# Optimization experiments

Measured on AMD Instinct MI355X. Metric: run time of the kernel, lower is better.

Reference implementation:

```python
import jax, jax.numpy as jnp
import numpy as np

NUM_GROUP, GROUP_SIZE = 128, 32
MASK = (64, 32, 32)
FEAT_DIM, N_POINTS = 1024, 2048
NBR_K = int(1.2 * GROUP_SIZE)  # int(nbr_ratio * group_size) = 38
SUPPORT, NBHD = 8, 32
W_RECON, W_MATCH, W_LATENT, W_MAN = 1.0, 1.0, 1.0, 0.1

gather = jax.vmap(lambda p, i: p[i])  # batched index_points

def sqdist(a, b):  # [B,M,3],[B,N,3] -> [B,M,N]
    return (jnp.sum(a * a, -1)[:, :, None] + jnp.sum(b * b, -1)[:, None, :]
            - 2.0 * jnp.einsum('bmd,bnd->bmn', a, b))

def knn_idx(q, db, k):  # indices into db of k nearest to each query
    return jax.lax.top_k(-sqdist(q, db), k)[1]

def fps(pts, G):  # farthest point sampling, [B,N,3] -> [B,G] indices
    b, n, _ = pts.shape
    def step(carry, _):
        min_d, far = carry
        cur = jnp.take_along_axis(pts, far[:, None, None], axis=1)
        min_d = jnp.minimum(min_d, jnp.sum((pts - cur) ** 2, -1))
        return (min_d, jnp.argmax(min_d, -1).astype(jnp.int32)), far
    init = (jnp.full((b, n), 1e10, dtype=pts.dtype), jnp.zeros((b,), jnp.int32))
    _, idxs = jax.lax.scan(step, init, None, length=G)
    return idxs.T

def bn(h, g, b_, m, v):  # BatchNorm1d, eval-mode running stats
    return (h - m) * jax.lax.rsqrt(v + 1e-5) * g + b_

def chamfer_l1(a, b):
    d = sqdist(a, b)
    d1 = jnp.sqrt(jnp.maximum(jnp.min(d, axis=2), 1e-12))
    d2 = jnp.sqrt(jnp.maximum(jnp.min(d, axis=1), 1e-12))
    return 0.5 * (d1.mean() + d2.mean())

def estimate_normals(xyz, K):  # PCA normal per point + direction disambiguation
    nb = gather(xyz, knn_idx(xyz, xyz, K))          # [B,N,K,3]
    c = nb - nb.mean(axis=2, keepdims=True)
    cov = jnp.einsum('bnki,bnkj->bnij', c, c) / K   # [B,N,3,3]
    _, v = jnp.linalg.eigh(cov)
    n = v[..., 0]                                   # smallest-eigenvalue eigvec
    proj = jnp.einsum('bnkd,bnd->bn', nb - xyz[:, :, None, :], n)
    return n * jnp.where(proj >= 0.0, 1.0, -1.0)[..., None]

def forward_all(pts, W1, b1, g1, be1, m1, v1, W2, b2, W3, b3, g2, be2, m2, v2,
                W4, b4, D1W, D1b, D2W, D2b, D3W, D3b, D4W, D4b):
    bsz = pts.shape[0]
    def encoder(x):  # PCN encoder: pointwise convs + global max pooling
        n = x.shape[1]
        h = jax.nn.relu(bn(x @ W1.T + b1, g1, be1, m1, v1))
        h = h @ W2.T + b2                           # [B,n,256]
        gmax = h.max(axis=1)
        h = jnp.concatenate([jnp.broadcast_to(gmax[:, None, :], (bsz, n, gmax.shape[-1])), h], axis=-1)
        h = jax.nn.relu(bn(h @ W3.T + b3, g2, be2, m2, v2))
        return (h @ W4.T + b4).max(axis=1)          # [B,FEAT_DIM]
    def decoder(z):
        h = jax.nn.relu(z @ D1W.T + D1b)
        h = jax.nn.relu(h @ D2W.T + D2b)
        h = jax.nn.relu(h @ D3W.T + D3b)
        return (h @ D4W.T + D4b).reshape(bsz, -1, 3)
    # --- Group divider: FPS centers + knn neighborhoods (centered) ---
    center = gather(pts, fps(pts, NUM_GROUP))       # [B,G,3]
    nbrs = gather(pts, knn_idx(center, pts, GROUP_SIZE)) - center[:, :, None, :]
    o1, o2 = MASK[0], MASK[0] + MASK[1]             # identity perm partition
    ng = (nbrs[:, :o1], nbrs[:, o1:o2], nbrs[:, o2:])
    cg = (center[:, :o1], center[:, o1:o2], center[:, o2:])
    rebuild0 = (ng[0] + cg[0][:, :, None, :]).reshape(bsz, -1, 3)
    feat = encoder(rebuild0)
    pred = decoder(feat)                            # [B,N_POINTS,3]
    # shape reconstruction loss
    idx = knn_idx(cg[0], pred, NBR_K)
    l_recon = W_RECON * chamfer_l1(rebuild0, gather(pred, idx).reshape(bsz, -1, 3))
    # shape matching loss
    rebuild1 = (ng[1] + cg[1][:, :, None, :]).reshape(bsz, -1, 3)
    idx = knn_idx(cg[1], pred, NBR_K)
    l_match = W_MATCH * chamfer_l1(rebuild1, gather(pred, idx).reshape(bsz, -1, 3))
    # latent reconstruction (detached input) - SmoothL1
    idx = knn_idx(cg[2], pred, GROUP_SIZE)
    feat_recon = encoder(jax.lax.stop_gradient(gather(pred, idx).reshape(bsz, -1, 3)))
    diff = feat - feat_recon
    ad = jnp.abs(diff)
    l_latent = W_LATENT * jnp.where(ad < 1.0, 0.5 * diff * diff, ad - 0.5).mean()
    # manifoldness (normal consistency) constraint
    normals = estimate_normals(pred, NBHD)
    nb = gather(normals, knn_idx(pred, pred, SUPPORT))  # [B,N,8,3]
    a = nb[:, :, :1, :]
    cos = jnp.sum(a * nb, -1) / (jnp.maximum(jnp.linalg.norm(a, axis=-1), 1e-6)
                                 * jnp.maximum(jnp.linalg.norm(nb, axis=-1), 1e-6))
    l_man = W_MAN * jnp.std(1.0 - cos, axis=-1, ddof=1).mean(axis=-1).mean()
    total = l_recon + l_match + l_latent + l_man
    return total, l_recon, l_match, l_latent, l_man


def setup_inputs() -> dict:
    ks = jax.random.split(jax.random.key(0), 10)
    rn = lambda k, sh: jax.random.normal(k, sh, jnp.float32) * 0.02
    z, o = jnp.zeros, jnp.ones
    return dict(
        pts=jax.random.normal(ks[0], (16, 2048, 3), jnp.float32),
        W1=rn(ks[1], (128, 3)), b1=z(128), g1=o(128), be1=z(128), m1=z(128), v1=o(128),
        W2=rn(ks[2], (256, 128)), b2=z(256),
        W3=rn(ks[3], (512, 512)), b3=z(512), g2=o(512), be2=z(512), m2=z(512), v2=o(512),
        W4=rn(ks[4], (FEAT_DIM, 512)), b4=z(FEAT_DIM),
        D1W=rn(ks[5], (2048, FEAT_DIM)), D1b=z(2048),
        D2W=rn(ks[6], (2048, 2048)), D2b=z(2048),
        D3W=rn(ks[7], (2048, 2048)), D3b=z(2048),
        D4W=rn(ks[8], (3 * N_POINTS, 2048)), D4b=z(3 * N_POINTS),
    )


def reference(pts, W1, b1, g1, be1, m1, v1, W2, b2, W3, b3, g2, be2, m2, v2,
              W4, b4, D1W, D1b, D2W, D2b, D3W, D3b, D4W, D4b):
    return forward_all(pts, W1, b1, g1, be1, m1, v1, W2, b2, W3, b3, g2, be2,
                       m2, v2, W4, b4, D1W, D1b, D2W, D2b, D3W, D3b, D4W, D4b)
```

## Files before the change

### kernel.cpp

```cpp
#include <hip/hip_runtime.h>
#include <math.h>

#define BSZ 16
#define NPTS 2048
#define NG 128
#define GS 32
#define NBRK 38

typedef _Float16 f16;
typedef _Float16 f16x8 __attribute__((ext_vector_type(8)));
typedef float f32x4 __attribute__((ext_vector_type(4)));

__device__ __forceinline__ unsigned fkey(float x) {
    unsigned u = __float_as_uint(x);
    return (u >> 31) ? ~u : (u | 0x80000000u);
}
__device__ __forceinline__ float fkey_inv(unsigned k) {
    unsigned u = (k >> 31) ? (k ^ 0x80000000u) : ~k;
    return __uint_as_float(u);
}

__device__ __forceinline__ unsigned wave_min_u32(unsigned v) {
    unsigned t;
    t = (unsigned)__builtin_amdgcn_update_dpp(-1, (int)v, 0x111, 0xF, 0xF, false);
    v = v < t ? v : t;
    t = (unsigned)__builtin_amdgcn_update_dpp(-1, (int)v, 0x112, 0xF, 0xF, false);
    v = v < t ? v : t;
    t = (unsigned)__builtin_amdgcn_update_dpp(-1, (int)v, 0x114, 0xF, 0xF, false);
    v = v < t ? v : t;
    t = (unsigned)__builtin_amdgcn_update_dpp(-1, (int)v, 0x118, 0xF, 0xF, false);
    v = v < t ? v : t;
    t = (unsigned)__builtin_amdgcn_update_dpp(-1, (int)v, 0x142, 0xA, 0xF, false);
    v = v < t ? v : t;
    t = (unsigned)__builtin_amdgcn_update_dpp(-1, (int)v, 0x143, 0xC, 0xF, false);
    v = v < t ? v : t;
    return (unsigned)__builtin_amdgcn_readlane((int)v, 63);
}

__device__ __forceinline__ unsigned long long wave_max_u64(unsigned long long v) {
#define DPPSTEP(ctrl, rmask)                                                                \
    {                                                                                       \
        unsigned tlo = (unsigned)__builtin_amdgcn_update_dpp(0, (int)(unsigned)v, ctrl,     \
                                                             rmask, 0xF, false);            \
        unsigned thi = (unsigned)__builtin_amdgcn_update_dpp(0, (int)(unsigned)(v >> 32),   \
                                                             ctrl, rmask, 0xF, false);      \
        unsigned long long t = ((unsigned long long)thi << 32) | tlo;                       \
        v = t > v ? t : v;                                                                  \
    }
    DPPSTEP(0x111, 0xF)
    DPPSTEP(0x112, 0xF)
    DPPSTEP(0x114, 0xF)
    DPPSTEP(0x118, 0xF)
    DPPSTEP(0x142, 0xA)
    DPPSTEP(0x143, 0xC)
#undef DPPSTEP
    unsigned rlo = (unsigned)__builtin_amdgcn_readlane((int)(unsigned)v, 63);
    unsigned rhi = (unsigned)__builtin_amdgcn_readlane((int)(unsigned)(v >> 32), 63);
    return ((unsigned long long)rhi << 32) | rlo;
}

__global__ __launch_bounds__(256, 1) void fps_kernel_v5(const float* __restrict__ pts,
                                                        float* __restrict__ center) {
    int b = blockIdx.x;
    const float* P = pts + (size_t)b * NPTS * 3;
    int tid = threadIdx.x;
    int lane = tid & 63, wave = tid >> 6;
    __shared__ __align__(16) float Pl[NPTS * 3];
    __shared__ __align__(16) float slot[2][4][8];
#pragma unroll
    for (int i = 0; i < 6; ++i) {
        int v4 = tid + i * 256;
        ((f32x4*)Pl)[v4] = ((const f32x4*)P)[v4];
    }
    __syncthreads();
    float px[8], py[8], pz[8], mind[8];
#pragma unroll
    for (int m = 0; m < 8; ++m) {
        int j = tid + (m << 8);
        px[m] = Pl[j * 3 + 0];
        py[m] = Pl[j * 3 + 1];
        pz[m] = Pl[j * 3 + 2];
        mind[m] = 1e10f;
    }
    float cx = Pl[0], cy = Pl[1], cz = Pl[2];
    float* C = center + (size_t)b * NG * 3;
#pragma unroll 1
    for (int g = 0; g < NG; ++g) {
        if (tid == 0) {
            C[g * 3 + 0] = cx; C[g * 3 + 1] = cy; C[g * 3 + 2] = cz;
        }
        if (g == NG - 1) break;
        float best0 = -1.f, best1 = -1.f;
        int bm0 = 0, bm1 = 1;
#pragma unroll
        for (int m = 0; m < 8; m += 2) {
            float dx0 = px[m] - cx, dy0 = py[m] - cy, dz0 = pz[m] - cz;
            float d0 = dx0 * dx0 + dy0 * dy0 + dz0 * dz0;
            float md0 = fminf(mind[m], d0);
            mind[m] = md0;
            if (md0 > best0) { best0 = md0; bm0 = m; }
            float dx1 = px[m + 1] - cx, dy1 = py[m + 1] - cy, dz1 = pz[m + 1] - cz;
            float d1 = dx1 * dx1 + dy1 * dy1 + dz1 * dz1;
            float md1 = fminf(mind[m + 1], d1);
            mind[m + 1] = md1;
            if (md1 > best1) { best1 = md1; bm1 = m + 1; }
        }
        bool t = (best1 > best0) || (best1 == best0 && bm1 < bm0);
        float bv = t ? best1 : best0;
        int bi = t ? bm1 : bm0;
        unsigned j = (unsigned)(tid + (bi << 8));
        unsigned long long key =
            ((unsigned long long)__float_as_uint(bv) << 32) | (unsigned)(~j);
        key = wave_max_u64(key);
        unsigned bj = ~(unsigned)key;
        int par = g & 1;
        if (lane < 3) slot[par][wave][2 + lane] = Pl[bj * 3 + lane];
        if (lane == 0) {
            slot[par][wave][0] = __uint_as_float((unsigned)key);
            slot[par][wave][1] = __uint_as_float((unsigned)(key >> 32));
        }
        __syncthreads();
        unsigned long long kb = 0ull;
        float nx = 0.f, ny = 0.f, nz = 0.f;
#pragma unroll
        for (int w = 0; w < 4; ++w) {
            f32x4 v = *(const f32x4*)&slot[par][w][0];
            float vz = slot[par][w][4];
            unsigned long long kk =
                ((unsigned long long)__float_as_uint(v[1]) << 32) | __float_as_uint(v[0]);
            bool tw = kk > kb;
            kb = tw ? kk : kb;
            nx = tw ? v[2] : nx;
            ny = tw ? v[3] : ny;
            nz = tw ? vz : nz;
        }
        cx = nx; cy = ny; cz = nz;
    }
}

__device__ __forceinline__ void knn_query(const float* __restrict__ q,
                                          const float* __restrict__ db,
                                          int k, int* __restrict__ o, int lane) {
    const unsigned KINF = 0xFFFFFFFFu;
    float qx = q[0], qy = q[1], qz = q[2];
    float qq = qx * qx + qy * qy + qz * qz;
    unsigned key[32];
    unsigned c0 = KINF, c1 = KINF, c2 = KINF, c3 = KINF;
#pragma unroll
    for (int m = 0; m < 32; ++m) {
        int j = lane + (m << 6);
        float bx = db[j * 3 + 0], by = db[j * 3 + 1], bz = db[j * 3 + 2];
        float dv = qq + bx * bx + by * by + bz * bz - 2.0f * (qx * bx + qy * by + qz * bz);
        unsigned qd = (unsigned)fminf(fmaxf(dv, 0.f) * 8192.0f, 2097151.f);
        unsigned kk = (qd << 11) | (unsigned)j;
        key[m] = kk;
        if (kk < c3) {
            if (kk < c2) {
                c3 = c2;
                if (kk < c1) {
                    c2 = c1;
                    if (kk < c0) { c1 = c0; c0 = kk; } else c1 = kk;
                } else c2 = kk;
            } else c3 = kk;
        }
    }
    unsigned hw = c3;
    int ncached = 4;
    for (int r = 0; r < k; ++r) {
        bool need = (c0 == KINF) && (ncached < 32);
        if (__any(need)) {
            unsigned best = KINF;
#pragma unroll
            for (int m = 0; m < 32; ++m) {
                unsigned v = key[m];
                best = (v > hw && v < best) ? v : best;
            }
            if (need) {
                c0 = best;
                hw = best;
                ncached = (best == KINF) ? 32 : ncached + 1;
            }
        }
        unsigned g = wave_min_u32(c0);
        if (lane == 0) o[r] = (int)(g & 0x7FFu);
        if (((g & 0x7FFu) & 63u) == (unsigned)lane) {
            c0 = c1; c1 = c2; c2 = c3; c3 = KINF;
        }
    }
}

__global__ void knn_kernel_v7(const float* __restrict__ Q, int q_bstride, int q_off, int nq,
                              const float* __restrict__ DB, int k,
                              int* __restrict__ out, int nbatch) {
    int wave = threadIdx.x >> 6, lane = threadIdx.x & 63;
    int qidx = blockIdx.x * 4 + wave;
    if (qidx >= nbatch * nq) return;
    int b = qidx / nq, qi = qidx % nq;
    knn_query(Q + ((size_t)b * q_bstride + q_off + qi) * 3,
              DB + (size_t)b * NPTS * 3, k, out + (size_t)qidx * k, lane);
}

__global__ void knn_post_kernel(const float* __restrict__ center,
                                const float* __restrict__ pred,
                                int* __restrict__ idxa, int* __restrict__ idxb,
                                int* __restrict__ idxc, int* __restrict__ knn32) {
    int wave = threadIdx.x >> 6, lane = threadIdx.x & 63;
    if (blockIdx.x < 512) {
        int qidx = blockIdx.x * 4 + wave;
        int b = qidx >> 7, qi = qidx & 127;
        const float* q = center + ((size_t)b * NG + qi) * 3;
        const float* db = pred + (size_t)b * NPTS * 3;
        int k; int* o;
        if (qi < 64) { k = NBRK; o = idxa + ((size_t)b * 64 + qi) * NBRK; }
        else if (qi < 96) { k = NBRK; o = idxb + ((size_t)b * 32 + qi - 64) * NBRK; }
        else { k = GS; o = idxc + ((size_t)b * 32 + qi - 96) * GS; }
        knn_query(q, db, k, o, lane);
    } else {
        int qidx = (blockIdx.x - 512) * 4 + wave;
        int b = qidx >> 11, qi = qidx & 2047;
        const float* db = pred + (size_t)b * NPTS * 3;
        knn_query(db + (size_t)qi * 3, db, GS, knn32 + (size_t)qidx * GS, lane);
    }
}

__global__ void gather_rebuild_kernel(const float* __restrict__ pts,
                                      const int* __restrict__ knnc,
                                      float* __restrict__ rebuild0,
                                      float* __restrict__ rebuild1) {
    int t = blockIdx.x * 256 + threadIdx.x;
    int s, tt; float* out;
    if (t < BSZ * 2048) {
        tt = t;
        int b = tt >> 11, j = tt & 2047;
        s = knnc[(size_t)b * (NG * GS) + j];
        out = rebuild0;
    } else {
        tt = t - BSZ * 2048;
        int b = tt >> 10, j = tt & 1023;
        s = knnc[(size_t)b * (NG * GS) + 2048 + j];
        out = rebuild1;
    }
    int b2 = (out == rebuild0) ? (tt >> 11) : (tt >> 10);
    const float* p = pts + ((size_t)b2 * NPTS + s) * 3;
    out[(size_t)tt * 3 + 0] = p[0];
    out[(size_t)tt * 3 + 1] = p[1];
    out[(size_t)tt * 3 + 2] = p[2];
}

__global__ void gather_abc_kernel(const float* __restrict__ pred,
                                  const int* __restrict__ idxa,
                                  const int* __restrict__ idxb,
                                  const int* __restrict__ idxc,
                                  float* __restrict__ gatha,
                                  float* __restrict__ gathb,
                                  float* __restrict__ gathc) {
    const int NA = BSZ * 2432, NB_ = BSZ * 1216, NC = BSZ * 1024;
    int t = blockIdx.x * 256 + threadIdx.x;
    const int* idx; int m, tt; float* out;
    if (t < NA) { tt = t; idx = idxa; m = 2432; out = gatha; }
    else if (t < NA + NB_) { tt = t - NA; idx = idxb; m = 1216; out = gathb; }
    else if (t < NA + NB_ + NC) { tt = t - NA - NB_; idx = idxc; m = 1024; out = gathc; }
    else return;
    int b = tt / m, j = tt - b * m;
    int s = idx[(size_t)b * m + j];
    const float* p = pred + ((size_t)b * NPTS + s) * 3;
    out[(size_t)tt * 3 + 0] = p[0];
    out[(size_t)tt * 3 + 1] = p[1];
    out[(size_t)tt * 3 + 2] = p[2];
}

__global__ void cvt_all_kernel(const float* __restrict__ W2, const float* __restrict__ W3,
                               const float* __restrict__ W4, f16* __restrict__ W2h,
                               f16* __restrict__ W3h, f16* __restrict__ W4h) {
    int t = blockIdx.x * 256 + threadIdx.x;
    if (t < 32768) {
        int n = t >> 7, k = t & 127;
        W2h[t] = (f16)W2[(size_t)n * 128 + k];
    } else if (t < 163840) {
        int u = t - 32768;
        int n = u >> 8, k = u & 255;
        W3h[u] = (f16)W3[(size_t)n * 512 + 256 + k];
    } else if (t < 688128) {
        int u = t - 163840;
        int n = u >> 9, k = u & 511;
        W4h[u] = (f16)W4[(size_t)n * 512 + k];
    }
}

__global__ void layer1_kernel(const float* __restrict__ X, const float* __restrict__ W1,
                              const float* __restrict__ b1, const float* __restrict__ g1,
                              const float* __restrict__ be1, const float* __restrict__ m1,
                              const float* __restrict__ v1, f16* __restrict__ H1, int M) {
    __shared__ float w[384], bb[128], sg[128], sb[128], sm[128], sv[128];
    for (int i = threadIdx.x; i < 384; i += 256) w[i] = W1[i];
    if (threadIdx.x < 128) {
        int c = threadIdx.x;
        bb[c] = b1[c]; sg[c] = g1[c]; sb[c] = be1[c]; sm[c] = m1[c]; sv[c] = v1[c];
    }
    __syncthreads();
    int t = blockIdx.x * 256 + threadIdx.x;
    if (t >= M * 16) return;
    int row = t >> 4, cg = (t & 15) * 8;
    float x0 = X[(size_t)row * 3], x1 = X[(size_t)row * 3 + 1], x2 = X[(size_t)row * 3 + 2];
    f16x8 outv;
#pragma unroll
    for (int j = 0; j < 8; ++j) {
        int c = cg + j;
        float tv = x0 * w[c * 3] + x1 * w[c * 3 + 1] + x2 * w[c * 3 + 2] + bb[c];
        float vv = (tv - sm[c]) * rsqrtf(sv[c] + 1e-5f) * sg[c] + sb[c];
        outv[j] = (f16)fmaxf(vv, 0.f);
    }
    *(f16x8*)&H1[(size_t)row * 128 + cg] = outv;
}

__global__ __launch_bounds__(256) void mfma_gemm_kernel(
        const f16* __restrict__ A, const f16* __restrict__ W, int K, int N,
        const float* __restrict__ bias, const float* __restrict__ bias2d,
        const float* __restrict__ bng, const float* __restrict__ bnb,
        const float* __restrict__ bnm, const float* __restrict__ bnv,
        f16* __restrict__ Cout, unsigned* __restrict__ maxkey,
        int rows_per_batch, int relu) {
    __shared__ f16 Als[128 * 40];
    __shared__ f16 Bls[128 * 40];
    int tid = threadIdx.x;
    int lane = tid & 63;
    int wave = tid >> 6;
    int wm = wave & 1, wn = wave >> 1;
    int c16 = lane & 15, quad = lane >> 4;
    int gx = gridDim.x;
    int nwg = gx * gridDim.y;
    int lin = blockIdx.y * gx + blockIdx.x;
    int qc = nwg >> 3, rc = nwg & 7;
    int xcd = lin & 7, pos = lin >> 3;
    int nlin = (xcd < rc ? xcd * (qc + 1) : rc * (qc + 1) + (xcd - rc) * qc) + pos;
    int row0 = (nlin / gx) * 128, col0 = (nlin % gx) * 128;
    int sr = tid >> 2;
    int skc = (tid & 3) * 8;

    f32x4 acc[4][4];
#pragma unroll
    for (int i = 0; i < 4; ++i)
#pragma unroll
        for (int j = 0; j < 4; ++j) acc[i][j] = (f32x4){0.f, 0.f, 0.f, 0.f};

    const f16* Ab = A + (size_t)(row0 + sr) * K + skc;
    const f16* Ab2 = A + (size_t)(row0 + sr + 64) * K + skc;
    const f16* Wb = W + (size_t)(col0 + sr) * K + skc;
    const f16* Wb2 = W + (size_t)(col0 + sr + 64) * K + skc;

    f16x8 pa0 = *(const f16x8*)Ab;
    f16x8 pa1 = *(const f16x8*)Ab2;
    f16x8 pb0 = *(const f16x8*)Wb;
    f16x8 pb1 = *(const f16x8*)Wb2;

    for (int k0 = 0; k0 < K; k0 += 32) {
        *(f16x8*)&Als[sr * 40 + skc] = pa0;
        *(f16x8*)&Als[(sr + 64) * 40 + skc] = pa1;
        *(f16x8*)&Bls[sr * 40 + skc] = pb0;
        *(f16x8*)&Bls[(sr + 64) * 40 + skc] = pb1;
        __syncthreads();
        if (k0 + 32 < K) {
            int kn = k0 + 32;
            pa0 = *(const f16x8*)(Ab + kn);
            pa1 = *(const f16x8*)(Ab2 + kn);
            pb0 = *(const f16x8*)(Wb + kn);
            pb1 = *(const f16x8*)(Wb2 + kn);
        }
        f16x8 af[4], bf[4];
#pragma unroll
        for (int s = 0; s < 4; ++s) {
            af[s] = *(const f16x8*)&Als[(wm * 64 + s * 16 + c16) * 40 + quad * 8];
            bf[s] = *(const f16x8*)&Bls[(wn * 64 + s * 16 + c16) * 40 + quad * 8];
        }
#pragma unroll
        for (int ms = 0; ms < 4; ++ms)
#pragma unroll
            for (int ns = 0; ns < 4; ++ns)
                acc[ms][ns] = __builtin_amdgcn_mfma_f32_16x16x32_f16(af[ms], bf[ns],
                                                                     acc[ms][ns], 0, 0, 0);
        __syncthreads();
    }

    int b = row0 / rows_per_batch;
#pragma unroll
    for (int ns = 0; ns < 4; ++ns) {
        int col = col0 + wn * 64 + ns * 16 + c16;
        float bv = bias ? bias[col] : 0.f;
        float b2v = bias2d ? bias2d[(size_t)b * N + col] : 0.f;
        float mx = -3e38f;
#pragma unroll
        for (int ms = 0; ms < 4; ++ms) {
#pragma unroll
            for (int j = 0; j < 4; ++j) {
                float v = acc[ms][ns][j] + bv + b2v;
                if (bng) v = (v - bnm[col]) * rsqrtf(bnv[col] + 1e-5f) * bng[col] + bnb[col];
                if (relu) v = fmaxf(v, 0.f);
                if (Cout)
                    Cout[(size_t)(row0 + wm * 64 + ms * 16 + quad * 4 + j) * N + col] = (f16)v;
                mx = fmaxf(mx, v);
            }
        }
        if (maxkey) {
            mx = fmaxf(mx, __shfl_xor(mx, 16, 64));
            mx = fmaxf(mx, __shfl_xor(mx, 32, 64));
            if (quad == 0) atomicMax(&maxkey[(size_t)b * N + col], fkey(mx));
        }
    }
}

__global__ void skinny_v2_kernel(const float* __restrict__ A, const float* __restrict__ W,
                                 int ldw, int woff, const float* __restrict__ bias,
                                 float* __restrict__ C, int K, int N, int relu, int akey) {
    int wave = threadIdx.x >> 6, lane = threadIdx.x & 63;
    int col = blockIdx.x * 4 + wave;
    if (col >= N) return;
    const float* w = W + (size_t)col * ldw + woff;
    float acc[16];
#pragma unroll
    for (int m = 0; m < 16; ++m) acc[m] = 0.f;
    for (int k0 = 0; k0 < K; k0 += 256) {
        f32x4 wv = *(const f32x4*)(w + k0 + lane * 4);
#pragma unroll
        for (int m = 0; m < 16; ++m) {
            f32x4 av = *(const f32x4*)(A + (size_t)m * K + k0 + lane * 4);
            if (akey) {
#pragma unroll
                for (int u = 0; u < 4; ++u) av[u] = fkey_inv(__float_as_uint(av[u]));
            }
            acc[m] += av[0] * wv[0] + av[1] * wv[1] + av[2] * wv[2] + av[3] * wv[3];
        }
    }
#pragma unroll
    for (int m = 0; m < 16; ++m)
#pragma unroll
        for (int s = 1; s < 64; s <<= 1) acc[m] += __shfl_xor(acc[m], s, 64);
    if (lane == 0) {
        float bv = bias[col];
#pragma unroll
        for (int m = 0; m < 16; ++m) {
            float v = acc[m] + bv;
            if (relu) v = fmaxf(v, 0.f);
            C[(size_t)m * N + col] = v;
        }
    }
}

__global__ void chamfer4_kernel(const float* __restrict__ rebuild0,
                                const float* __restrict__ gatha,
                                const float* __restrict__ rebuild1,
                                const float* __restrict__ gathb,
                                float* __restrict__ accum) {
    int blk = blockIdx.x;
    const float *A, *Bp; int na, nb, base; float* slot;
    if (blk < 1024)      { A = rebuild0; na = 2048; Bp = gatha;    nb = 2432; slot = accum + 0; base = 0; }
    else if (blk < 2240) { A = gatha;    na = 2432; Bp = rebuild0; nb = 2048; slot = accum + 1; base = 1024; }
    else if (blk < 2752) { A = rebuild1; na = 1024; Bp = gathb;    nb = 1216; slot = accum + 2; base = 2240; }
    else                 { A = gathb;    na = 1216; Bp = rebuild1; nb = 1024; slot = accum + 3; base = 2752; }
    int t = (blk - base) * 256 + threadIdx.x;
    int pt = t >> 3, sl = t & 7;
    float val = 0.f;
    if (pt < BSZ * na) {
        int b = pt / na;
        const float* a = A + (size_t)pt * 3;
        float ax = a[0], ay = a[1], az = a[2];
        float aa = ax * ax + ay * ay + az * az;
        const float* Bb = Bp + (size_t)b * nb * 3;
        float m = 3e38f;
        for (int j = sl; j < nb; j += 8) {
            float bx = Bb[j * 3 + 0], by = Bb[j * 3 + 1], bz = Bb[j * 3 + 2];
            float d = aa + bx * bx + by * by + bz * bz - 2.0f * (ax * bx + ay * by + az * bz);
            m = fminf(m, d);
        }
#pragma unroll
        for (int s = 1; s < 8; s <<= 1) m = fminf(m, __shfl_xor(m, s, 64));
        if (sl == 0) val = sqrtf(fmaxf(m, 1e-12f));
    }
    __shared__ float sdata[256];
    sdata[threadIdx.x] = val;
    __syncthreads();
    for (int s = 128; s > 0; s >>= 1) {
        if (threadIdx.x < s) sdata[threadIdx.x] += sdata[threadIdx.x + s];
        __syncthreads();
    }
    if (threadIdx.x == 0) atomicAdd(slot, sdata[0]);
}

__global__ void latent_kernel(const unsigned* __restrict__ k1,
                              const unsigned* __restrict__ k2,
                              int n, float* __restrict__ slot) {
    int t = blockIdx.x * blockDim.x + threadIdx.x;
    float val = 0.f;
    if (t < n) {
        float d = fkey_inv(k1[t]) - fkey_inv(k2[t]);
        float ad = fabsf(d);
        val = (ad < 1.f) ? (0.5f * d * d) : (ad - 0.5f);
    }
    __shared__ float sdata[256];
    sdata[threadIdx.x] = val;
    __syncthreads();
    for (int s = 128; s > 0; s >>= 1) {
        if (threadIdx.x < s) sdata[threadIdx.x] += sdata[threadIdx.x + s];
        __syncthreads();
    }
    if (threadIdx.x == 0) atomicAdd(slot, sdata[0]);
}

__device__ void smallest_evec(double cxx, double cxy, double cxz,
                              double cyy, double cyz, double czz, double ev[3]) {
    double p1 = cxy * cxy + cxz * cxz + cyz * cyz;
    double q = (cxx + cyy + czz) / 3.0;
    double p2 = (cxx - q) * (cxx - q) + (cyy - q) * (cyy - q) + (czz - q) * (czz - q) + 2.0 * p1;
    double lam = q;
    if (p2 > 0.0) {
        double p = sqrt(p2 / 6.0);
        double b00 = (cxx - q) / p, b11 = (cyy - q) / p, b22 = (czz - q) / p;
        double b01 = cxy / p, b02 = cxz / p, b12 = cyz / p;
        double detB = b00 * (b11 * b22 - b12 * b12) - b01 * (b01 * b22 - b12 * b02)
                    + b02 * (b01 * b12 - b11 * b02);
        double r = detB * 0.5;
        r = r < -1.0 ? -1.0 : (r > 1.0 ? 1.0 : r);
        double phi = acos(r) / 3.0;
        lam = q + 2.0 * p * cos(phi + 2.0943951023931953);
    }
    double r0x = cxx - lam, r0y = cxy, r0z = cxz;
    double r1x = cxy, r1y = cyy - lam, r1z = cyz;
    double r2x = cxz, r2y = cyz, r2z = czz - lam;
    double c0x = r0y * r1z - r0z * r1y, c0y = r0z * r1x - r0x * r1z, c0z = r0x * r1y - r0y * r1x;
    double c1x = r0y * r2z - r0z * r2y, c1y = r0z * r2x - r0x * r2z, c1z = r0x * r2y - r0y * r2x;
    double c2x = r1y * r2z - r1z * r2y, c2y = r1z * r2x - r1x * r2z, c2z = r1x * r2y - r1y * r2x;
    double n0 = c0x * c0x + c0y * c0y + c0z * c0z;
    double n1 = c1x * c1x + c1y * c1y + c1z * c1z;
    double n2 = c2x * c2x + c2y * c2y + c2z * c2z;
    double bx = c0x, by = c0y, bz = c0z, bn = n0;
    if (n1 > bn) { bx = c1x; by = c1y; bz = c1z; bn = n1; }
    if (n2 > bn) { bx = c2x; by = c2y; bz = c2z; bn = n2; }
    if (bn < 1e-280) { ev[0] = 1.0; ev[1] = 0.0; ev[2] = 0.0; return; }
    double inv = 1.0 / sqrt(bn);
    ev[0] = bx * inv; ev[1] = by * inv; ev[2] = bz * inv;
}

__global__ __launch_bounds__(64) void normals_kernel(const float* __restrict__ pred,
                                                     const int* __restrict__ knn,
                                                     float* __restrict__ nrm) {
    int t = blockIdx.x * 64 + threadIdx.x;
    if (t >= BSZ * NPTS) return;
    int b = t / NPTS, i = t % NPTS;
    const float* P = pred + (size_t)b * NPTS * 3;
    const int* id = knn + (size_t)t * 32;
    double sx = 0, sy = 0, sz = 0;
    double sxx = 0, sxy = 0, sxz = 0, syy = 0, syz = 0, szz = 0;
#pragma unroll
    for (int k0 = 0; k0 < 32; k0 += 4) {
        int4 jj = *(const int4*)&id[k0];
#pragma unroll
        for (int u = 0; u < 4; ++u) {
            int j = (u == 0) ? jj.x : (u == 1) ? jj.y : (u == 2) ? jj.z : jj.w;
            double x = (double)P[j * 3 + 0];
            double y = (double)P[j * 3 + 1];
            double z = (double)P[j * 3 + 2];
            sx += x; sy += y; sz += z;
            sxx += x * x; sxy += x * y; sxz += x * z;
            syy += y * y; syz += y * z; szz += z * z;
        }
    }
    double mx = sx * (1.0 / 32.0), my = sy * (1.0 / 32.0), mz = sz * (1.0 / 32.0);
    double cxx = sxx * (1.0 / 32.0) - mx * mx;
    double cxy = sxy * (1.0 / 32.0) - mx * my;
    double cxz = sxz * (1.0 / 32.0) - mx * mz;
    double cyy = syy * (1.0 / 32.0) - my * my;
    double cyz = syz * (1.0 / 32.0) - my * mz;
    double czz = szz * (1.0 / 32.0) - mz * mz;
    double ev[3];
    smallest_evec(cxx, cxy, cxz, cyy, cyz, czz, ev);
    float qx = P[i * 3 + 0], qy = P[i * 3 + 1], qz = P[i * 3 + 2];
    double proj = (sx - 32.0 * (double)qx) * ev[0] + (sy - 32.0 * (double)qy) * ev[1]
                + (sz - 32.0 * (double)qz) * ev[2];
    double s = (proj >= 0.0) ? 1.0 : -1.0;
    nrm[(size_t)t * 3 + 0] = (float)(ev[0] * s);
    nrm[(size_t)t * 3 + 1] = (float)(ev[1] * s);
    nrm[(size_t)t * 3 + 2] = (float)(ev[2] * s);
}

__global__ void manifold_kernel(const float* __restrict__ nrm, const int* __restrict__ knn,
                                int kstride, float* __restrict__ slot) {
    int t = blockIdx.x * blockDim.x + threadIdx.x;
    float val = 0.f;
    if (t < BSZ * NPTS) {
        int b = t / NPTS;
        const float* NB = nrm + (size_t)b * NPTS * 3;
        const int* id = knn + (size_t)t * kstride;
        int j0 = id[0];
        float ax = NB[j0 * 3 + 0], ay = NB[j0 * 3 + 1], az = NB[j0 * 3 + 2];
        float an = fmaxf(sqrtf(ax * ax + ay * ay + az * az), 1e-6f);
        float x[8]; float s = 0.f;
        for (int k = 0; k < 8; ++k) {
            int j = id[k];
            float bx = NB[j * 3 + 0], by = NB[j * 3 + 1], bz = NB[j * 3 + 2];
            float bn_ = fmaxf(sqrtf(bx * bx + by * by + bz * bz), 1e-6f);
            float c = (ax * bx + ay * by + az * bz) / (an * bn_);
            x[k] = 1.f - c; s += x[k];
        }
        float mean = s / 8.f;
        float var = 0.f;
        for (int k = 0; k < 8; ++k) { float d = x[k] - mean; var += d * d; }
        val = sqrtf(var / 7.f);
    }
    __shared__ float sdata[256];
    sdata[threadIdx.x] = val;
    __syncthreads();
    for (int s2 = 128; s2 > 0; s2 >>= 1) {
        if (threadIdx.x < s2) sdata[threadIdx.x] += sdata[threadIdx.x + s2];
        __syncthreads();
    }
    if (threadIdx.x == 0) atomicAdd(slot, sdata[0]);
}

__global__ void finalize_kernel(const float* __restrict__ acc, float* __restrict__ out) {
    float l_recon = 0.5f * (acc[0] / (16.f * 2048.f) + acc[1] / (16.f * 2432.f));
    float l_match = 0.5f * (acc[2] / (16.f * 1024.f) + acc[3] / (16.f * 1216.f));
    float l_latent = acc[4] / (16.f * 1024.f);
    float l_man = 0.1f * (acc[5] / (16.f * 2048.f));
    out[0] = l_recon + l_match + l_latent + l_man;
    out[1] = l_recon;
    out[2] = l_match;
    out[3] = l_latent;
    out[4] = l_man;
}

extern "C" void kernel_launch(void* const* d_in, const int* in_sizes, int n_in,
                              void* d_out, int out_size, void* d_ws, size_t ws_size,
                              hipStream_t stream) {
    (void)in_sizes; (void)n_in; (void)out_size; (void)ws_size;
    const float* pts = (const float*)d_in[0];
    const float* W1 = (const float*)d_in[1];
    const float* b1 = (const float*)d_in[2];
    const float* g1 = (const float*)d_in[3];
    const float* be1 = (const float*)d_in[4];
    const float* m1 = (const float*)d_in[5];
    const float* v1 = (const float*)d_in[6];
    const float* W2 = (const float*)d_in[7];
    const float* b2 = (const float*)d_in[8];
    const float* W3 = (const float*)d_in[9];
    const float* b3 = (const float*)d_in[10];
    const float* g2 = (const float*)d_in[11];
    const float* be2 = (const float*)d_in[12];
    const float* m2 = (const float*)d_in[13];
    const float* v2 = (const float*)d_in[14];
    const float* W4 = (const float*)d_in[15];
    const float* b4 = (const float*)d_in[16];
    const float* D1W = (const float*)d_in[17];
    const float* D1b = (const float*)d_in[18];
    const float* D2W = (const float*)d_in[19];
    const float* D2b = (const float*)d_in[20];
    const float* D3W = (const float*)d_in[21];
    const float* D3b = (const float*)d_in[22];
    const float* D4W = (const float*)d_in[23];
    const float* D4b = (const float*)d_in[24];

    char* ws = (char*)d_ws;
    size_t off = 0;
    auto alloc = [&](size_t bytes) -> void* {
        void* p = ws + off;
        off += (bytes + 255) & ~(size_t)255;
        return p;
    };
    float* center   = (float*)alloc((size_t)BSZ * NG * 3 * 4);
    int*   knnc     = (int*)  alloc((size_t)BSZ * NG * GS * 4);
    float* rebuild0 = (float*)alloc((size_t)BSZ * 2048 * 3 * 4);
    float* rebuild1 = (float*)alloc((size_t)BSZ * 1024 * 3 * 4);
    f16*   W2h      = (f16*)  alloc((size_t)256 * 128 * 2);
    f16*   W3h      = (f16*)  alloc((size_t)512 * 256 * 2);
    f16*   W4h      = (f16*)  alloc((size_t)1024 * 512 * 2);
    f16*   H1h      = (f16*)  alloc((size_t)BSZ * 2048 * 128 * 2);
    f16*   H2h      = (f16*)  alloc((size_t)BSZ * 2048 * 256 * 2);
    f16*   H3h      = (f16*)  alloc((size_t)BSZ * 2048 * 512 * 2);
    unsigned* keybase = (unsigned*)alloc(((size_t)BSZ * 2560 + 64) * 4);
    unsigned* gmaxkey1 = keybase;
    unsigned* gmaxkey2 = keybase + (size_t)BSZ * 256;
    unsigned* featkey1 = keybase + (size_t)BSZ * 512;
    unsigned* featkey2 = keybase + (size_t)BSZ * 512 + (size_t)BSZ * 1024;
    float* accum = (float*)(keybase + (size_t)BSZ * 2560);
    float* gpart    = (float*)alloc((size_t)BSZ * 512 * 4);
    float* dh1      = (float*)alloc((size_t)BSZ * 2048 * 4);
    float* dh2      = (float*)alloc((size_t)BSZ * 2048 * 4);
    float* dh3      = (float*)alloc((size_t)BSZ * 2048 * 4);
    float* pred     = (float*)alloc((size_t)BSZ * 6144 * 4);
    int*   idxa     = (int*)  alloc((size_t)BSZ * 64 * NBRK * 4);
    float* gatha    = (float*)alloc((size_t)BSZ * 64 * NBRK * 3 * 4);
    int*   idxb     = (int*)  alloc((size_t)BSZ * 32 * NBRK * 4);
    float* gathb    = (float*)alloc((size_t)BSZ * 32 * NBRK * 3 * 4);
    int*   idxc     = (int*)  alloc((size_t)BSZ * 32 * 32 * 4);
    float* gathc    = (float*)alloc((size_t)BSZ * 1024 * 3 * 4);
    int*   knn32    = (int*)  alloc((size_t)BSZ * 2048 * 32 * 4);
    float* nrmbuf   = (float*)alloc((size_t)BSZ * 2048 * 3 * 4);

    hipMemsetAsync(keybase, 0, ((size_t)BSZ * 2560 + 8) * 4, stream);

    cvt_all_kernel<<<2688, 256, 0, stream>>>(W2, W3, W4, W2h, W3h, W4h);

    fps_kernel_v5<<<BSZ, 256, 0, stream>>>(pts, center);
    knn_kernel_v7<<<(BSZ * NG + 3) / 4, 256, 0, stream>>>(center, NG, 0, NG, pts, GS,
                                                          knnc, BSZ);
    gather_rebuild_kernel<<<(BSZ * 3072) / 256, 256, 0, stream>>>(pts, knnc,
                                                                  rebuild0, rebuild1);

    auto enc = [&](const float* X, int n, unsigned* gkey, unsigned* fkeyout) {
        int M = BSZ * n;
        layer1_kernel<<<M / 16, 256, 0, stream>>>(X, W1, b1, g1, be1, m1, v1, H1h, M);
        mfma_gemm_kernel<<<dim3(256 / 128, M / 128), 256, 0, stream>>>(
            H1h, W2h, 128, 256, b2, nullptr, nullptr, nullptr, nullptr, nullptr,
            H2h, gkey, n, 0);
        skinny_v2_kernel<<<(512 + 3) / 4, 256, 0, stream>>>(
            (const float*)gkey, W3, 512, 0, b3, gpart, 256, 512, 0, 1);
        mfma_gemm_kernel<<<dim3(512 / 128, M / 128), 256, 0, stream>>>(
            H2h, W3h, 256, 512, nullptr, gpart, g2, be2, m2, v2, H3h, nullptr, n, 1);
        mfma_gemm_kernel<<<dim3(1024 / 128, M / 128), 256, 0, stream>>>(
            H3h, W4h, 512, 1024, b4, nullptr, nullptr, nullptr, nullptr, nullptr,
            nullptr, fkeyout, n, 0);
    };

    enc(rebuild0, 2048, gmaxkey1, featkey1);

    skinny_v2_kernel<<<2048 / 4, 256, 0, stream>>>((const float*)featkey1, D1W, 1024, 0,
                                                   D1b, dh1, 1024, 2048, 1, 1);
    skinny_v2_kernel<<<2048 / 4, 256, 0, stream>>>(dh1, D2W, 2048, 0, D2b, dh2,
                                                   2048, 2048, 1, 0);
    skinny_v2_kernel<<<2048 / 4, 256, 0, stream>>>(dh2, D3W, 2048, 0, D3b, dh3,
                                                   2048, 2048, 1, 0);
    skinny_v2_kernel<<<6144 / 4, 256, 0, stream>>>(dh3, D4W, 2048, 0, D4b, pred,
                                                   2048, 6144, 0, 0);

    knn_post_kernel<<<512 + (BSZ * NPTS) / 4, 256, 0, stream>>>(center, pred, idxa,
                                                                idxb, idxc, knn32);
    gather_abc_kernel<<<(BSZ * 4672) / 256, 256, 0, stream>>>(pred, idxa, idxb, idxc,
                                                              gatha, gathb, gathc);
    chamfer4_kernel<<<3360, 256, 0, stream>>>(rebuild0, gatha, rebuild1, gathb, accum);
    normals_kernel<<<(BSZ * NPTS) / 64, 64, 0, stream>>>(pred, knn32, nrmbuf);

    enc(gathc, 1024, gmaxkey2, featkey2);
    latent_kernel<<<(BSZ * 1024 + 255) / 256, 256, 0, stream>>>(featkey1, featkey2,
                                                                BSZ * 1024, accum + 4);
    manifold_kernel<<<(BSZ * 2048 + 255) / 256, 256, 0, stream>>>(nrmbuf, knn32, 32,
                                                                  accum + 5);

    finalize_kernel<<<1, 1, 0, stream>>>(accum, (float*)d_out);
}
```

Baseline: 752.4 us.

## Restructure chamfer with LDS-staged padded float4 points and precomputed norms

```diff
diff --git a/kernel.cpp b/kernel.cpp
--- a/kernel.cpp
+++ b/kernel.cpp
@@ -226,47 +226,63 @@
 __global__ void gather_rebuild_kernel(const float* __restrict__ pts,
                                       const int* __restrict__ knnc,
                                       float* __restrict__ rebuild0,
-                                      float* __restrict__ rebuild1) {
+                                      float* __restrict__ rebuild1,
+                                      f32x4* __restrict__ r0p4,
+                                      f32x4* __restrict__ r1p4) {
     int t = blockIdx.x * 256 + threadIdx.x;
-    int s, tt; float* out;
     if (t < BSZ * 2048) {
-        tt = t;
-        int b = tt >> 11, j = tt & 2047;
-        s = knnc[(size_t)b * (NG * GS) + j];
-        out = rebuild0;
+        int b = t >> 11, j = t & 2047;
+        int s = knnc[(size_t)b * (NG * GS) + j];
+        const float* p = pts + ((size_t)b * NPTS + s) * 3;
+        float x = p[0], y = p[1], z = p[2];
+        rebuild0[(size_t)t * 3 + 0] = x;
+        rebuild0[(size_t)t * 3 + 1] = y;
+        rebuild0[(size_t)t * 3 + 2] = z;
+        r0p4[t] = (f32x4){x, y, z, x * x + y * y + z * z};
     } else {
-        tt = t - BSZ * 2048;
+        int tt = t - BSZ * 2048;
         int b = tt >> 10, j = tt & 1023;
-        s = knnc[(size_t)b * (NG * GS) + 2048 + j];
-        out = rebuild1;
-    }
-    int b2 = (out == rebuild0) ? (tt >> 11) : (tt >> 10);
-    const float* p = pts + ((size_t)b2 * NPTS + s) * 3;
-    out[(size_t)tt * 3 + 0] = p[0];
-    out[(size_t)tt * 3 + 1] = p[1];
-    out[(size_t)tt * 3 + 2] = p[2];
+        int s = knnc[(size_t)b * (NG * GS) + 2048 + j];
+        const float* p = pts + ((size_t)b * NPTS + s) * 3;
+        float x = p[0], y = p[1], z = p[2];
+        rebuild1[(size_t)tt * 3 + 0] = x;
+        rebuild1[(size_t)tt * 3 + 1] = y;
+        rebuild1[(size_t)tt * 3 + 2] = z;
+        r1p4[tt] = (f32x4){x, y, z, x * x + y * y + z * z};
+    }
 }
 
 __global__ void gather_abc_kernel(const float* __restrict__ pred,
                                   const int* __restrict__ idxa,
                                   const int* __restrict__ idxb,
                                   const int* __restrict__ idxc,
-                                  float* __restrict__ gatha,
-                                  float* __restrict__ gathb,
+                                  f32x4* __restrict__ gap4,
+                                  f32x4* __restrict__ gbp4,
                                   float* __restrict__ gathc) {
     const int NA = BSZ * 2432, NB_ = BSZ * 1216, NC = BSZ * 1024;
     int t = blockIdx.x * 256 + threadIdx.x;
-    const int* idx; int m, tt; float* out;
-    if (t < NA) { tt = t; idx = idxa; m = 2432; out = gatha; }
-    else if (t < NA + NB_) { tt = t - NA; idx = idxb; m = 1216; out = gathb; }
-    else if (t < NA + NB_ + NC) { tt = t - NA - NB_; idx = idxc; m = 1024; out = gathc; }
-    else return;
-    int b = tt / m, j = tt - b * m;
-    int s = idx[(size_t)b * m + j];
-    const float* p = pred + ((size_t)b * NPTS + s) * 3;
-    out[(size_t)tt * 3 + 0] = p[0];
-    out[(size_t)tt * 3 + 1] = p[1];
-    out[(size_t)tt * 3 + 2] = p[2];
+    if (t < NA) {
+        int b = t / 2432, j = t - b * 2432;
+        int s = idxa[(size_t)b * 2432 + j];
+        const float* p = pred + ((size_t)b * NPTS + s) * 3;
+        float x = p[0], y = p[1], z = p[2];
+        gap4[t] = (f32x4){x, y, z, x * x + y * y + z * z};
+    } else if (t < NA + NB_) {
+        int tt = t - NA;
+        int b = tt / 1216, j = tt - b * 1216;
+        int s = idxb[(size_t)b * 1216 + j];
+        const float* p = pred + ((size_t)b * NPTS + s) * 3;
+        float x = p[0], y = p[1], z = p[2];
+        gbp4[tt] = (f32x4){x, y, z, x * x + y * y + z * z};
+    } else if (t < NA + NB_ + NC) {
+        int tt = t - NA - NB_;
+        int b = tt >> 10, j = tt & 1023;
+        int s = idxc[(size_t)b * 1024 + j];
+        const float* p = pred + ((size_t)b * NPTS + s) * 3;
+        gathc[(size_t)tt * 3 + 0] = p[0];
+        gathc[(size_t)tt * 3 + 1] = p[1];
+        gathc[(size_t)tt * 3 + 2] = p[2];
+    }
 }
 
 __global__ void cvt_all_kernel(const float* __restrict__ W2, const float* __restrict__ W3,
@@ -445,35 +461,43 @@
     }
 }
 
-__global__ void chamfer4_kernel(const float* __restrict__ rebuild0,
-                                const float* __restrict__ gatha,
-                                const float* __restrict__ rebuild1,
-                                const float* __restrict__ gathb,
-                                float* __restrict__ accum) {
+__global__ __launch_bounds__(256) void chamfer4_kernel(const f32x4* __restrict__ r0p4,
+                                                       const f32x4* __restrict__ gap4,
+                                                       const f32x4* __restrict__ r1p4,
+                                                       const f32x4* __restrict__ gbp4,
+                                                       float* __restrict__ accum) {
+    __shared__ __align__(16) float Bl[2432 * 4];
     int blk = blockIdx.x;
-    const float *A, *Bp; int na, nb, base; float* slot;
-    if (blk < 1024)      { A = rebuild0; na = 2048; Bp = gatha;    nb = 2432; slot = accum + 0; base = 0; }
-    else if (blk < 2240) { A = gatha;    na = 2432; Bp = rebuild0; nb = 2048; slot = accum + 1; base = 1024; }
-    else if (blk < 2752) { A = rebuild1; na = 1024; Bp = gathb;    nb = 1216; slot = accum + 2; base = 2240; }
-    else                 { A = gathb;    na = 1216; Bp = rebuild1; nb = 1024; slot = accum + 3; base = 2752; }
-    int t = (blk - base) * 256 + threadIdx.x;
-    int pt = t >> 3, sl = t & 7;
+    const f32x4 *A4, *B4; int na, nb, base, bpb; float* slot;
+    if (blk < 128)      { A4 = r0p4; na = 2048; B4 = gap4; nb = 2432; slot = accum + 0; base = 0;   bpb = 8; }
+    else if (blk < 288) { A4 = gap4; na = 2432; B4 = r0p4; nb = 2048; slot = accum + 1; base = 128; bpb = 10; }
+    else if (blk < 352) { A4 = r1p4; na = 1024; B4 = gbp4; nb = 1216; slot = accum + 2; base = 288; bpb = 4; }
+    else                { A4 = gbp4; na = 1216; B4 = r1p4; nb = 1024; slot = accum + 3; base = 352; bpb = 5; }
+    int rel = blk - base;
+    int b = rel / bpb, chunk = rel - b * bpb;
+    for (int i = threadIdx.x; i < nb; i += 256)
+        ((f32x4*)Bl)[i] = B4[(size_t)b * nb + i];
+    __syncthreads();
+    int aidx = chunk * 256 + threadIdx.x;
     float val = 0.f;
-    if (pt < BSZ * na) {
-        int b = pt / na;
-        const float* a = A + (size_t)pt * 3;
-        float ax = a[0], ay = a[1], az = a[2];
-        float aa = ax * ax + ay * ay + az * az;
-        const float* Bb = Bp + (size_t)b * nb * 3;
-        float m = 3e38f;
-        for (int j = sl; j < nb; j += 8) {
-            float bx = Bb[j * 3 + 0], by = Bb[j * 3 + 1], bz = Bb[j * 3 + 2];
-            float d = aa + bx * bx + by * by + bz * bz - 2.0f * (ax * bx + ay * by + az * bz);
-            m = fminf(m, d);
-        }
-#pragma unroll
-        for (int s = 1; s < 8; s <<= 1) m = fminf(m, __shfl_xor(m, s, 64));
-        if (sl == 0) val = sqrtf(fmaxf(m, 1e-12f));
+    if (aidx < na) {
+        f32x4 a = A4[(size_t)b * na + aidx];
+        float m2x = -2.f * a[0], m2y = -2.f * a[1], m2z = -2.f * a[2];
+        float m0 = 3e38f, m1 = 3e38f, m2 = 3e38f, m3 = 3e38f;
+        for (int j = 0; j < nb; j += 4) {
+            f32x4 b0 = ((const f32x4*)Bl)[j + 0];
+            f32x4 b1 = ((const f32x4*)Bl)[j + 1];
+            f32x4 b2 = ((const f32x4*)Bl)[j + 2];
+            f32x4 b3 = ((const f32x4*)Bl)[j + 3];
+            float t0 = fmaf(m2z, b0[2], fmaf(m2y, b0[1], fmaf(m2x, b0[0], b0[3])));
+            float t1 = fmaf(m2z, b1[2], fmaf(m2y, b1[1], fmaf(m2x, b1[0], b1[3])));
+            float t2 = fmaf(m2z, b2[2], fmaf(m2y, b2[1], fmaf(m2x, b2[0], b2[3])));
+            float t3 = fmaf(m2z, b3[2], fmaf(m2y, b3[1], fmaf(m2x, b3[0], b3[3])));
+            m0 = fminf(m0, t0); m1 = fminf(m1, t1);
+            m2 = fminf(m2, t2); m3 = fminf(m3, t3);
+        }
+        float m = fminf(fminf(m0, m1), fminf(m2, m3));
+        val = sqrtf(fmaxf(a[3] + m, 1e-12f));
     }
     __shared__ float sdata[256];
     sdata[threadIdx.x] = val;
@@ -668,6 +692,8 @@
     int*   knnc     = (int*)  alloc((size_t)BSZ * NG * GS * 4);
     float* rebuild0 = (float*)alloc((size_t)BSZ * 2048 * 3 * 4);
     float* rebuild1 = (float*)alloc((size_t)BSZ * 1024 * 3 * 4);
+    f32x4* r0p4     = (f32x4*)alloc((size_t)BSZ * 2048 * 16);
+    f32x4* r1p4     = (f32x4*)alloc((size_t)BSZ * 1024 * 16);
     f16*   W2h      = (f16*)  alloc((size_t)256 * 128 * 2);
     f16*   W3h      = (f16*)  alloc((size_t)512 * 256 * 2);
     f16*   W4h      = (f16*)  alloc((size_t)1024 * 512 * 2);
@@ -686,10 +712,10 @@
     float* dh3      = (float*)alloc((size_t)BSZ * 2048 * 4);
     float* pred     = (float*)alloc((size_t)BSZ * 6144 * 4);
     int*   idxa     = (int*)  alloc((size_t)BSZ * 64 * NBRK * 4);
-    float* gatha    = (float*)alloc((size_t)BSZ * 64 * NBRK * 3 * 4);
     int*   idxb     = (int*)  alloc((size_t)BSZ * 32 * NBRK * 4);
-    float* gathb    = (float*)alloc((size_t)BSZ * 32 * NBRK * 3 * 4);
     int*   idxc     = (int*)  alloc((size_t)BSZ * 32 * 32 * 4);
+    f32x4* gap4     = (f32x4*)alloc((size_t)BSZ * 2432 * 16);
+    f32x4* gbp4     = (f32x4*)alloc((size_t)BSZ * 1216 * 16);
     float* gathc    = (float*)alloc((size_t)BSZ * 1024 * 3 * 4);
     int*   knn32    = (int*)  alloc((size_t)BSZ * 2048 * 32 * 4);
     float* nrmbuf   = (float*)alloc((size_t)BSZ * 2048 * 3 * 4);
@@ -701,8 +727,8 @@
     fps_kernel_v5<<<BSZ, 256, 0, stream>>>(pts, center);
     knn_kernel_v7<<<(BSZ * NG + 3) / 4, 256, 0, stream>>>(center, NG, 0, NG, pts, GS,
                                                           knnc, BSZ);
-    gather_rebuild_kernel<<<(BSZ * 3072) / 256, 256, 0, stream>>>(pts, knnc,
-                                                                  rebuild0, rebuild1);
+    gather_rebuild_kernel<<<(BSZ * 3072) / 256, 256, 0, stream>>>(pts, knnc, rebuild0,
+                                                                  rebuild1, r0p4, r1p4);
 
     auto enc = [&](const float* X, int n, unsigned* gkey, unsigned* fkeyout) {
         int M = BSZ * n;
@@ -733,8 +759,8 @@
     knn_post_kernel<<<512 + (BSZ * NPTS) / 4, 256, 0, stream>>>(center, pred, idxa,
                                                                 idxb, idxc, knn32);
     gather_abc_kernel<<<(BSZ * 4672) / 256, 256, 0, stream>>>(pred, idxa, idxb, idxc,
-                                                              gatha, gathb, gathc);
-    chamfer4_kernel<<<3360, 256, 0, stream>>>(rebuild0, gatha, rebuild1, gathb, accum);
+                                                              gap4, gbp4, gathc);
+    chamfer4_kernel<<<432, 256, 0, stream>>>(r0p4, gap4, r1p4, gbp4, accum);
     normals_kernel<<<(BSZ * NPTS) / 64, 64, 0, stream>>>(pred, knn32, nrmbuf);
 
     enc(gathc, 1024, gmaxkey2, featkey2);
```

New measurement: 665.1 us. 11.6% less time.
